# Kernel optimization log

Hardware: AMD Instinct MI355X
Metric: run time of the kernel (lower is better)

Reference implementation:

```python
import jax, jax.numpy as jnp
import numpy as np

B, S, D = 2, 2048, 2048
H, KV, HD = 16, 4, 128          # n_heads, n_kv_heads, head_dim = d_model // n_heads
R = H // KV                      # n_rep (GQA group size)
THETA = 500000.0


def _rotate_half(x):
    x1, x2 = jnp.split(x, 2, axis=-1)
    return jnp.concatenate([-x2, x1], axis=-1)


def _rope_cos_sin(position_ids):
    # inv_freq over even dims, outer with positions, duplicated (LLaMA-style)
    inv_freq = 1.0 / (THETA ** (jnp.arange(0, HD, 2, dtype=jnp.float32) / HD))
    freqs = position_ids.astype(jnp.float32)[..., None] * inv_freq  # (B, S, HD/2)
    emb = jnp.concatenate([freqs, freqs], axis=-1)                  # (B, S, HD)
    return jnp.cos(emb)[:, None], jnp.sin(emb)[:, None]             # (B, 1, S, HD)


def setup_inputs() -> dict:
    key = jax.random.key(0)
    ks = jax.random.split(key, 5)
    x = jax.random.normal(ks[0], (B, S, D), dtype=jnp.float32)
    wq = jax.random.normal(ks[1], (D, H * HD), dtype=jnp.float32) * (D ** -0.5)
    wk = jax.random.normal(ks[2], (D, KV * HD), dtype=jnp.float32) * (D ** -0.5)
    wv = jax.random.normal(ks[3], (D, KV * HD), dtype=jnp.float32) * (D ** -0.5)
    wo = jax.random.normal(ks[4], (H * HD, D), dtype=jnp.float32) * (D ** -0.5)
    causal = jnp.tril(jnp.ones((S, S), dtype=bool))
    attn_mask = jnp.where(causal, 0.0, -1e9).astype(jnp.float32)[None, None]  # (1,1,S,S)
    position_ids = jnp.tile(jnp.arange(S, dtype=jnp.int32)[None, :], (B, 1))
    return {"x": x, "wq": wq, "wk": wk, "wv": wv, "wo": wo,
            "attn_mask": attn_mask, "position_ids": position_ids}


def reference(x, wq, wk, wv, wo, attn_mask, position_ids):
    b, s, _ = x.shape
    # projections (bias-free Linear) + head split, (B, heads, S, HD)
    q = (x @ wq).reshape(b, s, H, HD).transpose(0, 2, 1, 3)
    k = (x @ wk).reshape(b, s, KV, HD).transpose(0, 2, 1, 3)
    v = (x @ wv).reshape(b, s, KV, HD).transpose(0, 2, 1, 3)
    cos, sin = _rope_cos_sin(position_ids)
    q = q * cos + _rotate_half(q) * sin
    k = k * cos + _rotate_half(k) * sin
    # GQA: group q heads (B, KV, R, S, HD); equivalent to repeat_interleave on K/V
    qg = q.reshape(b, KV, R, s, HD)
    scores = jnp.einsum('bgrsd,bgtd->bgrst', qg.astype(jnp.float32),
                        k.astype(jnp.float32)) / np.float32(np.sqrt(HD))
    scores = scores + attn_mask[:, :, None]          # (1,1,1,S,S) broadcast
    p = jax.nn.softmax(scores, axis=-1).astype(x.dtype)
    out = jnp.einsum('bgrst,bgtd->bgrsd', p, v)      # (B, KV, R, S, HD)
    out = out.reshape(b, H, s, HD).transpose(0, 2, 1, 3).reshape(b, s, H * HD)
    return out @ wo
```

## Files before the change

### kernel.cpp

```cpp
#include <hip/hip_runtime.h>
#include <hip/hip_bf16.h>
#include <math.h>

#define Bsz 2
#define Sq  2048
#define Dm  2048
#define Hn  16
#define KVn 4
#define HDn 128

typedef __attribute__((ext_vector_type(8))) short bf16x8;
typedef __attribute__((ext_vector_type(4))) float f32x4;

__device__ __forceinline__ short f2b(float f) {
    __hip_bfloat16 h = __float2bfloat16(f);
    return *reinterpret_cast<short*>(&h);
}
__device__ __forceinline__ float b2f(short s) {
    __hip_bfloat16 h = *reinterpret_cast<__hip_bfloat16*>(&s);
    return __bfloat162float(h);
}

__global__ __launch_bounds__(256) void f2b_kernel(
    const float* __restrict__ X, short* __restrict__ Y, int n4)
{
    int i = blockIdx.x * 256 + threadIdx.x;
    if (i >= n4) return;
    float4 v = ((const float4*)X)[i];
    short4 o;
    o.x = f2b(v.x); o.y = f2b(v.y); o.z = f2b(v.z); o.w = f2b(v.w);
    ((short4*)Y)[i] = o;
}

__global__ __launch_bounds__(256) void wconv_all_kernel(
    const float* __restrict__ wq, const float* __restrict__ wk,
    const float* __restrict__ wv, const float* __restrict__ wo,
    short* __restrict__ wqkvT, short* __restrict__ woT)
{
    __shared__ float t[32][33];
    const int n0 = blockIdx.x * 32;
    const int k0 = blockIdx.y * 32;
    const int tx = threadIdx.x, ty = threadIdx.y;

    const float* W; int Nsec, nloc; short* dst;
    if (n0 < 2048)      { W = wq; Nsec = 2048; nloc = n0;        dst = wqkvT + (size_t)n0 * Dm; }
    else if (n0 < 2560) { W = wk; Nsec = 512;  nloc = n0 - 2048; dst = wqkvT + (size_t)n0 * Dm; }
    else if (n0 < 3072) { W = wv; Nsec = 512;  nloc = n0 - 2560; dst = wqkvT + (size_t)n0 * Dm; }
    else                { W = wo; Nsec = 2048; nloc = n0 - 3072; dst = woT + (size_t)(n0 - 3072) * Dm; }

#pragma unroll
    for (int r = 0; r < 4; ++r) {
        const int row = ty + 8 * r;
        t[row][tx] = W[(size_t)(k0 + row) * Nsec + nloc + tx];
    }
    __syncthreads();
#pragma unroll
    for (int r = 0; r < 4; ++r) {
        const int row = ty + 8 * r;
        dst[(size_t)row * Dm + k0 + tx] = f2b(t[tx][row]);
    }
}

template <typename OT>
__global__ __launch_bounds__(256) void gemm_bt_kernel(
    const short* __restrict__ A, const short* __restrict__ Bt,
    OT* __restrict__ C, int M, int N, int K)
{
    __shared__ __align__(16) short As[128 * 64];
    __shared__ __align__(16) short Bs[128 * 64];

    const int tid  = threadIdx.x;
    const int w    = tid >> 6;
    const int lane = tid & 63;
    const int m16  = lane & 15;
    const int g4   = lane >> 4;
    const int wm   = w >> 1, wn = w & 1;

    const int row0 = blockIdx.y * 128;
    const int col0 = blockIdx.x * 128;

    const short* Ab = A  + (size_t)row0 * K;
    const short* Bb = Bt + (size_t)col0 * K;

    const int trow = tid >> 3;
    const int soct = (tid & 7) ^ (trow & 7);

    f32x4 acc[4][4];
#pragma unroll
    for (int i = 0; i < 4; ++i)
#pragma unroll
        for (int j = 0; j < 4; ++j) acc[i][j] = (f32x4){0.f, 0.f, 0.f, 0.f};

    for (int k0 = 0; k0 < K; k0 += 64) {
#pragma unroll
        for (int r = 0; r < 4; ++r) {
            const short* gp = Ab + (size_t)(r * 32 + trow) * K + k0 + soct * 8;
            short* lp = &As[(size_t)(r * 256 + w * 64) * 8];
            __builtin_amdgcn_global_load_lds(
                (const __attribute__((address_space(1))) void*)gp,
                (__attribute__((address_space(3))) void*)lp, 16, 0, 0);
        }
#pragma unroll
        for (int r = 0; r < 4; ++r) {
            const short* gp = Bb + (size_t)(r * 32 + trow) * K + k0 + soct * 8;
            short* lp = &Bs[(size_t)(r * 256 + w * 64) * 8];
            __builtin_amdgcn_global_load_lds(
                (const __attribute__((address_space(1))) void*)gp,
                (__attribute__((address_space(3))) void*)lp, 16, 0, 0);
        }
        __syncthreads();

#pragma unroll
        for (int kc = 0; kc < 2; ++kc) {
            bf16x8 a[4], b[4];
            const int swz = (kc * 4 + g4) ^ (m16 & 7);
#pragma unroll
            for (int s = 0; s < 4; ++s) {
                const int rowA = wm * 64 + s * 16 + m16;
                a[s] = *(const bf16x8*)&As[rowA * 64 + swz * 8];
                const int rowB = wn * 64 + s * 16 + m16;
                b[s] = *(const bf16x8*)&Bs[rowB * 64 + swz * 8];
            }
#pragma unroll
            for (int i = 0; i < 4; ++i)
#pragma unroll
                for (int j = 0; j < 4; ++j)
                    acc[i][j] = __builtin_amdgcn_mfma_f32_16x16x32_bf16(
                        a[i], b[j], acc[i][j], 0, 0, 0);
        }
        __syncthreads();
    }

#pragma unroll
    for (int i = 0; i < 4; ++i) {
        const int mbase = row0 + wm * 64 + i * 16 + g4 * 4;
#pragma unroll
        for (int j = 0; j < 4; ++j) {
            const int n = col0 + wn * 64 + j * 16 + m16;
#pragma unroll
            for (int r = 0; r < 4; ++r) {
                if constexpr (sizeof(OT) == 2)
                    C[(size_t)(mbase + r) * N + n] = f2b(acc[i][j][r]);
                else
                    C[(size_t)(mbase + r) * N + n] = acc[i][j][r];
            }
        }
    }
}

__global__ __launch_bounds__(256) void rope_all_kernel(
    const short* __restrict__ C3b, short* __restrict__ Qb, short* __restrict__ Kb,
    const int* __restrict__ pos_ids, float qscale, int total)
{
    int idx = blockIdx.x * blockDim.x + threadIdx.x;
    if (idx >= total) return;
    const int i = idx & 63;
    int rest = idx >> 6;
    const int s = rest % Sq;
    const int b = rest / Sq;

    const int pos = pos_ids[b * Sq + s];
    const float e   = -(float)(2 * i) * (1.0f / (float)HDn);
    const float inv = exp2f(e * 18.931568569324174f);
    const float f   = (float)pos * inv;
    float sn, c;
    sincosf(f, &sn, &c);

    const short* src = C3b + ((size_t)(b * Sq + s)) * 3072;

#pragma unroll
    for (int h = 0; h < Hn; ++h) {
        const float x1 = b2f(src[h * HDn + i]);
        const float x2 = b2f(src[h * HDn + i + 64]);
        const size_t dst = (((size_t)b * Hn + h) * Sq + s) * HDn;
        Qb[dst + i]      = f2b((x1 * c - x2 * sn) * qscale);
        Qb[dst + i + 64] = f2b((x2 * c + x1 * sn) * qscale);
    }
#pragma unroll
    for (int h = 0; h < KVn; ++h) {
        const float x1 = b2f(src[2048 + h * HDn + i]);
        const float x2 = b2f(src[2048 + h * HDn + i + 64]);
        const size_t dst = (((size_t)b * KVn + h) * Sq + s) * HDn;
        Kb[dst + i]      = f2b(x1 * c - x2 * sn);
        Kb[dst + i + 64] = f2b(x2 * c + x1 * sn);
    }
}

__global__ __launch_bounds__(256) void vconv_kernel(
    const short* __restrict__ C3b, short* __restrict__ Vt)
{
    __shared__ short t[32][34];
    const int bk = blockIdx.z;
    const int b  = bk >> 2, kv = bk & 3;
    const int s0 = blockIdx.x * 32;
    const int d0 = blockIdx.y * 32;
    const int tx = threadIdx.x, ty = threadIdx.y;

#pragma unroll
    for (int r = 0; r < 4; ++r) {
        const int row = ty + 8 * r;
        t[row][tx] = C3b[((size_t)(b * Sq + s0 + row)) * 3072 + 2560 + kv * HDn + d0 + tx];
    }
    __syncthreads();
#pragma unroll
    for (int r = 0; r < 4; ++r) {
        const int row = ty + 8 * r;
        Vt[((size_t)bk * HDn + d0 + row) * Sq + s0 + tx] = t[tx][row];
    }
}

__global__ __launch_bounds__(256, 2) void fattn_kernel(
    const short* __restrict__ Qb, const short* __restrict__ Kb,
    const short* __restrict__ Vtb, short* __restrict__ AOb)
{
    __shared__ __align__(16) short Ks[2][64 * 128];
    __shared__ __align__(16) short Vs[2][128 * 64];

    const int tid  = threadIdx.x;
    const int w    = tid >> 6;
    const int lane = tid & 63;
    const int m16  = lane & 15;
    const int g4   = lane >> 4;

    const int p  = blockIdx.x & 15;
    const int h  = (blockIdx.x >> 4) & 15;
    const int b  = blockIdx.x >> 8;
    const int kv = h >> 2;

    const int htA = 31 - p, htB = p;
    const int nchA = htA + 1, nchB = htB + 1;
    const int qbA = htA << 6, qbB = htB << 6;

    bf16x8 qfA[4], qfB[4];
    {
        const short* qpA = Qb + (((size_t)b * Hn + h) * Sq + qbA + w * 16 + m16) * HDn + g4 * 8;
        const short* qpB = Qb + (((size_t)b * Hn + h) * Sq + qbB + w * 16 + m16) * HDn + g4 * 8;
#pragma unroll
        for (int c = 0; c < 4; ++c) {
            qfA[c] = *(const bf16x8*)(qpA + c * 32);
            qfB[c] = *(const bf16x8*)(qpB + c * 32);
        }
    }

    const short* kbase = Kb  + ((size_t)b * KVn + kv) * Sq * HDn;
    const short* vbase = Vtb + ((size_t)b * KVn + kv) * (size_t)HDn * Sq;

    const short* gpK[4];
    const short* gpV[4];
#pragma unroll
    for (int r = 0; r < 4; ++r) {
        const int ci = r * 256 + tid;
        const int R  = ci >> 4, o = ci & 15;
        const int hf = (R >> 5) & 1, Rl = R & 31;
        const int phys = hf * 32 + ((Rl >> 2) & 3) * 8 + ((Rl >> 4) & 1) * 4 + (Rl & 3);
        gpK[r] = kbase + (size_t)phys * HDn + (o ^ (R & 7)) * 8;
        const int d = ci >> 3, ov = ci & 7;
        gpV[r] = vbase + (size_t)d * Sq + (ov ^ (d & 7)) * 8;
    }

    auto stage = [&](int ktE, int buf) {
#pragma unroll
        for (int r = 0; r < 4; ++r) {
            const short* gp = gpK[r] + (size_t)ktE * HDn;
            short* lp = &Ks[buf][(size_t)(r * 256 + w * 64) * 8];
            __builtin_amdgcn_global_load_lds(
                (const __attribute__((address_space(1))) void*)gp,
                (__attribute__((address_space(3))) void*)lp, 16, 0, 0);
        }
#pragma unroll
        for (int r = 0; r < 4; ++r) {
            const short* gp = gpV[r] + ktE;
            short* lp = &Vs[buf][(size_t)(r * 256 + w * 64) * 8];
            __builtin_amdgcn_global_load_lds(
                (const __attribute__((address_space(1))) void*)gp,
                (__attribute__((address_space(3))) void*)lp, 16, 0, 0);
        }
    };

    f32x4 Ot[8];
#pragma unroll
    for (int t = 0; t < 8; ++t) Ot[t] = (f32x4){0.f, 0.f, 0.f, 0.f};
    float mcur = -1e30f, lcur = 0.f;
    int gpar = 0;

    auto run_job = [&](const bf16x8 (&qf)[4], int nch, int qb, bool lastJob) {
        for (int ch = 0; ch < nch; ++ch) {
            const int cur = gpar & 1;
            gpar ^= 1;
            const int kt = ch << 6;

            __syncthreads();
            if (ch + 1 < nch)      stage((ch + 1) << 6, cur ^ 1);
            else if (!lastJob)     stage(0, cur ^ 1);

            const bool diag = (ch == nch - 1);
            const short* KsC = Ks[cur];
            const short* VsC = Vs[cur];

            f32x4 sc[4];
            __builtin_amdgcn_s_setprio(1);
#pragma unroll
            for (int f = 0; f < 4; ++f) {
                f32x4 a = (f32x4){0.f, 0.f, 0.f, 0.f};
                const int krow = f * 16 + m16;
#pragma unroll
                for (int c = 0; c < 4; ++c) {
                    bf16x8 kf = *(const bf16x8*)&KsC[krow * 128 + (((c * 4 + g4) ^ (m16 & 7)) * 8)];
                    a = __builtin_amdgcn_mfma_f32_16x16x32_bf16(kf, qf[c], a, 0, 0, 0);
                }
                sc[f] = a;
            }
            __builtin_amdgcn_s_setprio(0);

            if (diag) {
                const int qg = qb + w * 16 + m16;
#pragma unroll
                for (int f = 0; f < 4; ++f)
#pragma unroll
                    for (int ii = 0; ii < 4; ++ii) {
                        const int kg = kt + (f >> 1) * 32 + g4 * 8 + (f & 1) * 4 + ii;
                        if (kg > qg) sc[f][ii] = -1e30f;
                    }
            }

            float mx = sc[0][0];
#pragma unroll
            for (int f = 0; f < 4; ++f)
#pragma unroll
                for (int ii = 0; ii < 4; ++ii) mx = fmaxf(mx, sc[f][ii]);
            mx = fmaxf(mx, __shfl_xor(mx, 16));
            mx = fmaxf(mx, __shfl_xor(mx, 32));
            if (!__all(mx <= mcur + 8.0f)) {
                const float nm = fmaxf(mcur, mx);
                const float alpha = exp2f(mcur - nm);
                mcur = nm;
                lcur *= alpha;
#pragma unroll
                for (int t = 0; t < 8; ++t)
#pragma unroll
                    for (int ii = 0; ii < 4; ++ii) Ot[t][ii] *= alpha;
            }
            float ps = 0.f;
#pragma unroll
            for (int f = 0; f < 4; ++f)
#pragma unroll
                for (int ii = 0; ii < 4; ++ii) {
                    sc[f][ii] = exp2f(sc[f][ii] - mcur);
                    ps += sc[f][ii];
                }
            ps += __shfl_xor(ps, 16);
            ps += __shfl_xor(ps, 32);
            lcur += ps;

            bf16x8 pf[2];
#pragma unroll
            for (int hf = 0; hf < 2; ++hf) {
                bf16x8 pk;
#pragma unroll
                for (int j8 = 0; j8 < 8; ++j8)
                    pk[j8] = f2b(j8 < 4 ? sc[hf * 2][j8] : sc[hf * 2 + 1][j8 - 4]);
                pf[hf] = pk;
            }

            __builtin_amdgcn_s_setprio(1);
#pragma unroll
            for (int t = 0; t < 8; ++t) {
                const int d = t * 16 + m16;
                bf16x8 vfa = *(const bf16x8*)&VsC[d * 64 + ((g4 ^ (d & 7)) * 8)];
                bf16x8 vfb = *(const bf16x8*)&VsC[d * 64 + (((4 + g4) ^ (d & 7)) * 8)];
                Ot[t] = __builtin_amdgcn_mfma_f32_16x16x32_bf16(vfa, pf[0], Ot[t], 0, 0, 0);
                Ot[t] = __builtin_amdgcn_mfma_f32_16x16x32_bf16(vfb, pf[1], Ot[t], 0, 0, 0);
            }
            __builtin_amdgcn_s_setprio(0);
        }
    };

    auto writeO = [&](int qb) {
        const float inv = 1.0f / lcur;
        short* op = AOb + ((size_t)(b * Sq + qb + w * 16 + m16)) * (Hn * HDn) + h * HDn + g4 * 4;
#pragma unroll
        for (int t = 0; t < 8; ++t) {
            short4 o;
            o.x = f2b(Ot[t][0] * inv);
            o.y = f2b(Ot[t][1] * inv);
            o.z = f2b(Ot[t][2] * inv);
            o.w = f2b(Ot[t][3] * inv);
            *(short4*)(op + t * 16) = o;
        }
    };

    stage(0, 0);
    run_job(qfA, nchA, qbA, false);
    writeO(qbA);
#pragma unroll
    for (int t = 0; t < 8; ++t) Ot[t] = (f32x4){0.f, 0.f, 0.f, 0.f};
    mcur = -1e30f; lcur = 0.f;
    run_job(qfB, nchB, qbB, true);
    writeO(qbB);
}

extern "C" void kernel_launch(void* const* d_in, const int* in_sizes, int n_in,
                              void* d_out, int out_size, void* d_ws, size_t ws_size,
                              hipStream_t stream)
{
    const float* x   = (const float*)d_in[0];
    const float* wq  = (const float*)d_in[1];
    const float* wk  = (const float*)d_in[2];
    const float* wv  = (const float*)d_in[3];
    const float* wo  = (const float*)d_in[4];
    const int* pos   = (const int*)d_in[6];
    float* out = (float*)d_out;

    const int M = Bsz * Sq;
    const size_t nX  = (size_t)M * Dm;

    short* xb    = (short*)d_ws;
    short* wqkvT = xb + nX;
    short* woT   = wqkvT + (size_t)3072 * Dm;
    short* C3b   = woT + (size_t)Dm * Dm;
    short* Qb    = C3b + (size_t)M * 3072;
    short* Kb    = Qb + nX;
    short* Vtb   = Kb + (size_t)Bsz * KVn * Sq * HDn;
    short* AOb   = Vtb + (size_t)Bsz * KVn * Sq * HDn;

    f2b_kernel<<<(nX / 4 + 255) / 256, 256, 0, stream>>>(x, xb, nX / 4);
    wconv_all_kernel<<<dim3(5120 / 32, Dm / 32), dim3(32, 8), 0, stream>>>(
        wq, wk, wv, wo, wqkvT, woT);

    gemm_bt_kernel<short><<<dim3(3072 / 128, M / 128), 256, 0, stream>>>(
        xb, wqkvT, C3b, M, 3072, Dm);

    {
        const float qscale = 0.08838834764831845f * 1.4426950408889634f;
        int tot = Bsz * Sq * 64;
        rope_all_kernel<<<(tot + 255) / 256, 256, 0, stream>>>(
            C3b, Qb, Kb, pos, qscale, tot);
    }
    vconv_kernel<<<dim3(Sq / 32, HDn / 32, Bsz * KVn), dim3(32, 8), 0, stream>>>(
        C3b, Vtb);

    fattn_kernel<<<Bsz * Hn * (Sq / 128), 256, 0, stream>>>(Qb, Kb, Vtb, AOb);

    gemm_bt_kernel<float><<<dim3(Dm / 128, M / 128), 256, 0, stream>>>(
        AOb, woT, out, M, Dm, Dm);
}
```

Baseline: 323.8 us.

## Fuse paired causal query tiles into one 32x32 MFMA pass over K/V

The attention kernel now uses 32x32x16 MFMAs. Each wave's 32 lanes hold 16 rows from the late query tile and 16 from the early one, so both tiles share a single sweep over the K/V chunks instead of two separate sweeps. The early tile's output is written once its diagonal chunk is done. Its lanes keep computing discarded values for later chunks. Softmax probabilities are packed with v_cvt_pk_bf16_f32. This roughly halves K/V staging and LDS reads per block and lowers loop overhead, at the cost of larger accumulators (more VGPR pressure) and some wasted lanes.

```diff
diff --git a/kernel.cpp b/kernel.cpp
--- a/kernel.cpp
+++ b/kernel.cpp
@@ -11,6 +11,8 @@
 
 typedef __attribute__((ext_vector_type(8))) short bf16x8;
 typedef __attribute__((ext_vector_type(4))) float f32x4;
+typedef __attribute__((ext_vector_type(16))) float f32x16;
+typedef __attribute__((ext_vector_type(4))) unsigned int u32x4;
 
 __device__ __forceinline__ short f2b(float f) {
     __hip_bfloat16 h = __float2bfloat16(f);
@@ -19,6 +21,11 @@
 __device__ __forceinline__ float b2f(short s) {
     __hip_bfloat16 h = *reinterpret_cast<__hip_bfloat16*>(&s);
     return __bfloat162float(h);
+}
+__device__ __forceinline__ unsigned pk2(float lo, float hh) {
+    unsigned r;
+    asm("v_cvt_pk_bf16_f32 %0, %1, %2" : "=v"(r) : "v"(lo), "v"(hh));
+    return r;
 }
 
 __global__ __launch_bounds__(256) void f2b_kernel(
@@ -219,27 +226,28 @@
     const int tid  = threadIdx.x;
     const int w    = tid >> 6;
     const int lane = tid & 63;
-    const int m16  = lane & 15;
-    const int g4   = lane >> 4;
-
-    const int p  = blockIdx.x & 15;
-    const int h  = (blockIdx.x >> 4) & 15;
-    const int b  = blockIdx.x >> 8;
-    const int kv = h >> 2;
-
-    const int htA = 31 - p, htB = p;
-    const int nchA = htA + 1, nchB = htB + 1;
-    const int qbA = htA << 6, qbB = htB << 6;
-
-    bf16x8 qfA[4], qfB[4];
+    const int l31  = lane & 31;
+    const int hi   = lane >> 5;
+
+    const int i    = blockIdx.x;
+    const int half = i >> 8;
+    const int k4   = i & 15;
+    const int p    = half ? k4 : 15 - k4;
+    const int h    = (i >> 4) & 15;
+    const int b    = i >> 8;
+    const int kv   = h >> 2;
+
+    const int nch = 32 - p;
+    const int qAb = (31 - p) * 64;
+    const int qBb = p * 64;
+    const int isB = l31 >> 4;
+    const int qg  = (isB ? qBb : qAb) + w * 16 + (l31 & 15);
+
+    bf16x8 qf[8];
     {
-        const short* qpA = Qb + (((size_t)b * Hn + h) * Sq + qbA + w * 16 + m16) * HDn + g4 * 8;
-        const short* qpB = Qb + (((size_t)b * Hn + h) * Sq + qbB + w * 16 + m16) * HDn + g4 * 8;
-#pragma unroll
-        for (int c = 0; c < 4; ++c) {
-            qfA[c] = *(const bf16x8*)(qpA + c * 32);
-            qfB[c] = *(const bf16x8*)(qpB + c * 32);
-        }
+        const short* qp = Qb + (((size_t)b * Hn + h) * Sq + qg) * HDn + hi * 8;
+#pragma unroll
+        for (int c = 0; c < 8; ++c) qf[c] = *(const bf16x8*)(qp + c * 16);
     }
 
     const short* kbase = Kb  + ((size_t)b * KVn + kv) * Sq * HDn;
@@ -277,126 +285,139 @@
         }
     };
 
-    f32x4 Ot[8];
-#pragma unroll
-    for (int t = 0; t < 8; ++t) Ot[t] = (f32x4){0.f, 0.f, 0.f, 0.f};
+    f32x16 Ot[4];
+#pragma unroll
+    for (int dc = 0; dc < 4; ++dc)
+#pragma unroll
+        for (int e = 0; e < 16; ++e) Ot[dc][e] = 0.f;
     float mcur = -1e30f, lcur = 0.f;
-    int gpar = 0;
-
-    auto run_job = [&](const bf16x8 (&qf)[4], int nch, int qb, bool lastJob) {
-        for (int ch = 0; ch < nch; ++ch) {
-            const int cur = gpar & 1;
-            gpar ^= 1;
-            const int kt = ch << 6;
-
-            __syncthreads();
-            if (ch + 1 < nch)      stage((ch + 1) << 6, cur ^ 1);
-            else if (!lastJob)     stage(0, cur ^ 1);
-
-            const bool diag = (ch == nch - 1);
-            const short* KsC = Ks[cur];
-            const short* VsC = Vs[cur];
-
-            f32x4 sc[4];
-            __builtin_amdgcn_s_setprio(1);
-#pragma unroll
-            for (int f = 0; f < 4; ++f) {
-                f32x4 a = (f32x4){0.f, 0.f, 0.f, 0.f};
-                const int krow = f * 16 + m16;
-#pragma unroll
-                for (int c = 0; c < 4; ++c) {
-                    bf16x8 kf = *(const bf16x8*)&KsC[krow * 128 + (((c * 4 + g4) ^ (m16 & 7)) * 8)];
-                    a = __builtin_amdgcn_mfma_f32_16x16x32_bf16(kf, qf[c], a, 0, 0, 0);
+
+    stage(0, 0);
+
+    for (int ch = 0; ch < nch; ++ch) {
+        const int cur = ch & 1;
+        const int ktb = ch << 6;
+
+        __syncthreads();
+        if (ch + 1 < nch) stage((ch + 1) << 6, cur ^ 1);
+
+        const short* KsC = Ks[cur];
+        const short* VsC = Vs[cur];
+
+        f32x16 s0, s1;
+#pragma unroll
+        for (int e = 0; e < 16; ++e) { s0[e] = 0.f; s1[e] = 0.f; }
+        __builtin_amdgcn_s_setprio(1);
+        {
+            const int swz = l31 & 7;
+#pragma unroll
+            for (int c = 0; c < 8; ++c) {
+                const int oc = ((2 * c + hi) ^ swz) * 8;
+                bf16x8 k0 = *(const bf16x8*)&KsC[l31 * 128 + oc];
+                bf16x8 k1 = *(const bf16x8*)&KsC[(32 + l31) * 128 + oc];
+                s0 = __builtin_amdgcn_mfma_f32_32x32x16_bf16(k0, qf[c], s0, 0, 0, 0);
+                s1 = __builtin_amdgcn_mfma_f32_32x32x16_bf16(k1, qf[c], s1, 0, 0, 0);
+            }
+        }
+        __builtin_amdgcn_s_setprio(0);
+
+        if (ch == p || ch == nch - 1) {
+#pragma unroll
+            for (int r = 0; r < 16; ++r) {
+                const int koff = ktb + 8 * hi + 16 * ((r >> 2) & 1) + 4 * (r >> 3) + (r & 3);
+                if (koff > qg)      s0[r] = -1e30f;
+                if (koff + 32 > qg) s1[r] = -1e30f;
+            }
+        }
+
+        float mx = -1e30f;
+#pragma unroll
+        for (int r = 0; r < 16; ++r) mx = fmaxf(mx, fmaxf(s0[r], s1[r]));
+        mx = fmaxf(mx, __shfl_xor(mx, 32));
+        if (!__all(mx <= mcur + 8.0f)) {
+            const float nm = fmaxf(mcur, mx);
+            const float al = exp2f(mcur - nm);
+            mcur = nm; lcur *= al;
+#pragma unroll
+            for (int dc = 0; dc < 4; ++dc)
+#pragma unroll
+                for (int e = 0; e < 16; ++e) Ot[dc][e] *= al;
+        }
+        float psa = 0.f, psb = 0.f;
+#pragma unroll
+        for (int r = 0; r < 16; ++r) {
+            s0[r] = exp2f(s0[r] - mcur); psa += s0[r];
+            s1[r] = exp2f(s1[r] - mcur); psb += s1[r];
+        }
+        float ps = psa + psb;
+        ps += __shfl_xor(ps, 32);
+        lcur += ps;
+
+        bf16x8 pb0, pb1, pb2, pb3;
+        {
+            u32x4 u;
+            u[0] = pk2(s0[0],  s0[1]);  u[1] = pk2(s0[2],  s0[3]);
+            u[2] = pk2(s0[8],  s0[9]);  u[3] = pk2(s0[10], s0[11]);
+            pb0 = *(bf16x8*)&u;
+            u[0] = pk2(s0[4],  s0[5]);  u[1] = pk2(s0[6],  s0[7]);
+            u[2] = pk2(s0[12], s0[13]); u[3] = pk2(s0[14], s0[15]);
+            pb1 = *(bf16x8*)&u;
+            u[0] = pk2(s1[0],  s1[1]);  u[1] = pk2(s1[2],  s1[3]);
+            u[2] = pk2(s1[8],  s1[9]);  u[3] = pk2(s1[10], s1[11]);
+            pb2 = *(bf16x8*)&u;
+            u[0] = pk2(s1[4],  s1[5]);  u[1] = pk2(s1[6],  s1[7]);
+            u[2] = pk2(s1[12], s1[13]); u[3] = pk2(s1[14], s1[15]);
+            pb3 = *(bf16x8*)&u;
+        }
+
+        __builtin_amdgcn_s_setprio(1);
+#pragma unroll
+        for (int dc = 0; dc < 4; ++dc) {
+            const int dR  = dc * 32 + l31;
+            const int swz = l31 & 7;
+            bf16x8 v0 = *(const bf16x8*)&VsC[dR * 64 + (((0 + hi) ^ swz) * 8)];
+            bf16x8 v1 = *(const bf16x8*)&VsC[dR * 64 + (((2 + hi) ^ swz) * 8)];
+            bf16x8 v2 = *(const bf16x8*)&VsC[dR * 64 + (((4 + hi) ^ swz) * 8)];
+            bf16x8 v3 = *(const bf16x8*)&VsC[dR * 64 + (((6 + hi) ^ swz) * 8)];
+            Ot[dc] = __builtin_amdgcn_mfma_f32_32x32x16_bf16(v0, pb0, Ot[dc], 0, 0, 0);
+            Ot[dc] = __builtin_amdgcn_mfma_f32_32x32x16_bf16(v1, pb1, Ot[dc], 0, 0, 0);
+            Ot[dc] = __builtin_amdgcn_mfma_f32_32x32x16_bf16(v2, pb2, Ot[dc], 0, 0, 0);
+            Ot[dc] = __builtin_amdgcn_mfma_f32_32x32x16_bf16(v3, pb3, Ot[dc], 0, 0, 0);
+        }
+        __builtin_amdgcn_s_setprio(0);
+
+        if (ch == p && isB) {
+            const float inv = 1.0f / lcur;
+            short* op = AOb + ((size_t)(b * Sq + qg)) * (Hn * HDn) + h * HDn + 4 * hi;
+#pragma unroll
+            for (int dc = 0; dc < 4; ++dc)
+#pragma unroll
+                for (int j = 0; j < 4; ++j) {
+                    short4 o;
+                    o.x = f2b(Ot[dc][4 * j + 0] * inv);
+                    o.y = f2b(Ot[dc][4 * j + 1] * inv);
+                    o.z = f2b(Ot[dc][4 * j + 2] * inv);
+                    o.w = f2b(Ot[dc][4 * j + 3] * inv);
+                    *(short4*)(op + dc * 32 + 8 * j) = o;
                 }
-                sc[f] = a;
+        }
+    }
+
+    if (!isB) {
+        const float inv = 1.0f / lcur;
+        short* op = AOb + ((size_t)(b * Sq + qg)) * (Hn * HDn) + h * HDn + 4 * hi;
+#pragma unroll
+        for (int dc = 0; dc < 4; ++dc)
+#pragma unroll
+            for (int j = 0; j < 4; ++j) {
+                short4 o;
+                o.x = f2b(Ot[dc][4 * j + 0] * inv);
+                o.y = f2b(Ot[dc][4 * j + 1] * inv);
+                o.z = f2b(Ot[dc][4 * j + 2] * inv);
+                o.w = f2b(Ot[dc][4 * j + 3] * inv);
+                *(short4*)(op + dc * 32 + 8 * j) = o;
             }
-            __builtin_amdgcn_s_setprio(0);
-
-            if (diag) {
-                const int qg = qb + w * 16 + m16;
-#pragma unroll
-                for (int f = 0; f < 4; ++f)
-#pragma unroll
-                    for (int ii = 0; ii < 4; ++ii) {
-                        const int kg = kt + (f >> 1) * 32 + g4 * 8 + (f & 1) * 4 + ii;
-                        if (kg > qg) sc[f][ii] = -1e30f;
-                    }
-            }
-
-            float mx = sc[0][0];
-#pragma unroll
-            for (int f = 0; f < 4; ++f)
-#pragma unroll
-                for (int ii = 0; ii < 4; ++ii) mx = fmaxf(mx, sc[f][ii]);
-            mx = fmaxf(mx, __shfl_xor(mx, 16));
-            mx = fmaxf(mx, __shfl_xor(mx, 32));
-            if (!__all(mx <= mcur + 8.0f)) {
-                const float nm = fmaxf(mcur, mx);
-                const float alpha = exp2f(mcur - nm);
-                mcur = nm;
-                lcur *= alpha;
-#pragma unroll
-                for (int t = 0; t < 8; ++t)
-#pragma unroll
-                    for (int ii = 0; ii < 4; ++ii) Ot[t][ii] *= alpha;
-            }
-            float ps = 0.f;
-#pragma unroll
-            for (int f = 0; f < 4; ++f)
-#pragma unroll
-                for (int ii = 0; ii < 4; ++ii) {
-                    sc[f][ii] = exp2f(sc[f][ii] - mcur);
-                    ps += sc[f][ii];
-                }
-            ps += __shfl_xor(ps, 16);
-            ps += __shfl_xor(ps, 32);
-            lcur += ps;
-
-            bf16x8 pf[2];
-#pragma unroll
-            for (int hf = 0; hf < 2; ++hf) {
-                bf16x8 pk;
-#pragma unroll
-                for (int j8 = 0; j8 < 8; ++j8)
-                    pk[j8] = f2b(j8 < 4 ? sc[hf * 2][j8] : sc[hf * 2 + 1][j8 - 4]);
-                pf[hf] = pk;
-            }
-
-            __builtin_amdgcn_s_setprio(1);
-#pragma unroll
-            for (int t = 0; t < 8; ++t) {
-                const int d = t * 16 + m16;
-                bf16x8 vfa = *(const bf16x8*)&VsC[d * 64 + ((g4 ^ (d & 7)) * 8)];
-                bf16x8 vfb = *(const bf16x8*)&VsC[d * 64 + (((4 + g4) ^ (d & 7)) * 8)];
-                Ot[t] = __builtin_amdgcn_mfma_f32_16x16x32_bf16(vfa, pf[0], Ot[t], 0, 0, 0);
-                Ot[t] = __builtin_amdgcn_mfma_f32_16x16x32_bf16(vfb, pf[1], Ot[t], 0, 0, 0);
-            }
-            __builtin_amdgcn_s_setprio(0);
-        }
-    };
-
-    auto writeO = [&](int qb) {
-        const float inv = 1.0f / lcur;
-        short* op = AOb + ((size_t)(b * Sq + qb + w * 16 + m16)) * (Hn * HDn) + h * HDn + g4 * 4;
-#pragma unroll
-        for (int t = 0; t < 8; ++t) {
-            short4 o;
-            o.x = f2b(Ot[t][0] * inv);
-            o.y = f2b(Ot[t][1] * inv);
-            o.z = f2b(Ot[t][2] * inv);
-            o.w = f2b(Ot[t][3] * inv);
-            *(short4*)(op + t * 16) = o;
-        }
-    };
-
-    stage(0, 0);
-    run_job(qfA, nchA, qbA, false);
-    writeO(qbA);
-#pragma unroll
-    for (int t = 0; t < 8; ++t) Ot[t] = (f32x4){0.f, 0.f, 0.f, 0.f};
-    mcur = -1e30f; lcur = 0.f;
-    run_job(qfB, nchB, qbB, true);
-    writeO(qbB);
+    }
 }
 
 extern "C" void kernel_launch(void* const* d_in, const int* in_sizes, int n_in,
@@ -439,7 +460,7 @@
     vconv_kernel<<<dim3(Sq / 32, HDn / 32, Bsz * KVn), dim3(32, 8), 0, stream>>>(
         C3b, Vtb);
 
-    fattn_kernel<<<Bsz * Hn * (Sq / 128), 256, 0, stream>>>(Qb, Kb, Vtb, AOb);
+    fattn_kernel<<<Bsz * Hn * 16, 256, 0, stream>>>(Qb, Kb, Vtb, AOb);
 
     gemm_bt_kernel<float><<<dim3(Dm / 128, M / 128), 256, 0, stream>>>(
         AOb, woT, out, M, Dm, Dm);
```

Result: slower. 345.3 us (+6.6%).
